# Kernel tuning notes

Hardware: AMD Instinct MI355X
Metric: run time of the kernel (lower is better)

The kernel has to match this reference:

```python
import jax, jax.numpy as jnp
import numpy as np

D_MODEL = 768
D_STATE = 16
GRID = 3
B, L = 2, 2048


def setup_inputs() -> dict:
    key = jax.random.key(0)
    ks = jax.random.split(key, 16)
    d, n, g = D_MODEL, D_STATE, GRID
    s = lambda fan: 1.0 / np.sqrt(fan)
    return {
        "x": jax.random.normal(ks[0], (B, L, d), jnp.float32),
        "priority_map": jax.random.uniform(ks[1], (B, L), jnp.float32),
        "W_in": jax.random.normal(ks[2], (d, 2 * d), jnp.float32) * s(d),
        "b_in": jnp.zeros((2 * d,), jnp.float32),
        "ln_g": jnp.ones((d,), jnp.float32),
        "ln_b": jnp.zeros((d,), jnp.float32),
        "kd_base": jax.random.normal(ks[3], (d, d), jnp.float32) * s(d),
        "kd_spline": jax.random.normal(ks[4], (d, g, d), jnp.float32) * s(d * g),
        "kb_base": jax.random.normal(ks[5], (d, n), jnp.float32) * s(d),
        "kb_spline": jax.random.normal(ks[6], (d, g, n), jnp.float32) * s(d * g),
        "kc_base": jax.random.normal(ks[7], (d, n), jnp.float32) * s(d),
        "kc_spline": jax.random.normal(ks[8], (d, g, n), jnp.float32) * s(d * g),
        "A_log": jax.random.uniform(ks[9], (d, n), jnp.float32, 1.0, 5.0),
        "D_param": jnp.ones((d,), jnp.float32),
        "W_out": jax.random.normal(ks[10], (d, d), jnp.float32) * s(d),
        "b_out": jnp.zeros((d,), jnp.float32),
    }


def _kan_dense(x, w_base, w_spline, grid):
    # FastKAN-style: SiLU base branch + Gaussian-RBF spline branch over grid_size centers.
    base = jnp.einsum("bld,do->blo", jax.nn.silu(x), w_base)
    phi = jnp.exp(-((x[..., None] - grid) ** 2))          # [B,L,D,G]
    spline = jnp.einsum("bldg,dgo->blo", phi, w_spline)
    return base + spline


def _layernorm(x, g, b, eps=1e-5):
    mu = jnp.mean(x, axis=-1, keepdims=True)
    var = jnp.mean((x - mu) ** 2, axis=-1, keepdims=True)
    return (x - mu) * jax.lax.rsqrt(var + eps) * g + b


def reference(x, priority_map, W_in, b_in, ln_g, ln_b, kd_base, kd_spline,
              kb_base, kb_spline, kc_base, kc_spline, A_log, D_param, W_out, b_out):
    grid = jnp.linspace(-1.0, 1.0, GRID).astype(x.dtype)
    xz = x @ W_in + b_in
    x_proj, z = jnp.split(xz, 2, axis=-1)                  # [B,L,D] each
    x_norm = _layernorm(x_proj, ln_g, ln_b)

    delta = jax.nn.softplus(_kan_dense(x_norm, kd_base, kd_spline, grid))  # [B,L,D]
    delta = delta * jnp.exp(-priority_map)[..., None]      # inverse priority modulation

    Bmat = _kan_dense(x_norm, kb_base, kb_spline, grid)    # [B,L,N]
    Cmat = _kan_dense(x_norm, kc_base, kc_spline, grid)    # [B,L,N]

    A_cont = -jnp.exp(A_log)                               # [D,N]
    dA = jnp.exp(jnp.einsum("bld,dn->bldn", delta, A_cont))       # [B,L,D,N]
    dBx = jnp.einsum("bld,bln->bldn", delta, Bmat) * x_proj[..., None]

    def combine(c1, c2):
        a1, b1 = c1
        a2, b2 = c2
        return a1 * a2, a2 * b1 + b2

    _, h = jax.lax.associative_scan(combine, (dA, dBx), axis=1)    # h: [B,L,D,N]

    y = jnp.einsum("bln,bldn->bld", Cmat, h) + D_param * x_proj
    y = y * jax.nn.silu(z)
    return y @ W_out + b_out
```

## Files before the change

### kernel.cpp

```cpp
#include <hip/hip_runtime.h>
#include <math.h>
#include <stdint.h>

#define D_MODEL 768
#define D_STATE 16
#define BB      2
#define LL      2048
#define MM      (BB * LL)
#define NC      64
#define CL      (LL / NC)
#define SLD     896

typedef __attribute__((ext_vector_type(8))) short short8;
typedef __attribute__((ext_vector_type(4))) float f32x4;

__device__ __forceinline__ short f2bf(float f) {
    union { float f; uint32_t u; } v; v.f = f;
    uint32_t r = v.u + 0x7fff + ((v.u >> 16) & 1);
    return (short)(r >> 16);
}
__device__ __forceinline__ float silu(float x) {
    return x / (1.0f + __expf(-x));
}

#define LDK 40

__global__ __launch_bounds__(256)
void gemm_bf16(const short* __restrict__ A,
               const short* __restrict__ Bt,
               const float* __restrict__ bias,
               const float* __restrict__ prio,
               float* __restrict__ C,
               int M, int N, int K)
{
    __shared__ short As[128 * LDK];
    __shared__ short Bs[128 * LDK];

    int tid  = threadIdx.x;
    int wid  = tid >> 6, lane = tid & 63;
    int wr   = wid >> 1, wc = wid & 1;
    int row0 = blockIdx.y * 128;
    int col0 = blockIdx.x * 128;

    f32x4 acc[4][4] = {};

    int fr = lane & 15;
    int kb = (lane >> 4) * 8;

    for (int k0 = 0; k0 < K; k0 += 32) {
        short8 av[2], bv[2];
        #pragma unroll
        for (int e = 0; e < 2; ++e) {
            int flat = tid + e * 256;
            int r  = flat >> 2;
            int cc = (flat & 3) * 8;
            av[e] = *(const short8*)(A  + (size_t)(row0 + r) * K + k0 + cc);
            bv[e] = *(const short8*)(Bt + (size_t)(col0 + r) * K + k0 + cc);
        }
        __syncthreads();
        #pragma unroll
        for (int e = 0; e < 2; ++e) {
            int flat = tid + e * 256;
            int r  = flat >> 2;
            int cc = (flat & 3) * 8;
            *(short8*)(&As[r * LDK + cc]) = av[e];
            *(short8*)(&Bs[r * LDK + cc]) = bv[e];
        }
        __syncthreads();

        short8 af[4], bf[4];
        #pragma unroll
        for (int m = 0; m < 4; ++m)
            af[m] = *(const short8*)(&As[(wr * 64 + m * 16 + fr) * LDK + kb]);
        #pragma unroll
        for (int n = 0; n < 4; ++n)
            bf[n] = *(const short8*)(&Bs[(wc * 64 + n * 16 + fr) * LDK + kb]);
        #pragma unroll
        for (int m = 0; m < 4; ++m)
            #pragma unroll
            for (int n = 0; n < 4; ++n)
                acc[m][n] = __builtin_amdgcn_mfma_f32_16x16x32_bf16(
                                af[m], bf[n], acc[m][n], 0, 0, 0);
    }

    int rq = lane >> 4;
    #pragma unroll
    for (int m = 0; m < 4; ++m) {
        #pragma unroll
        for (int n = 0; n < 4; ++n) {
            int col = col0 + wc * 64 + n * 16 + fr;
            float bvv = bias ? bias[col] : 0.0f;
            #pragma unroll
            for (int r = 0; r < 4; ++r) {
                int row = row0 + wr * 64 + m * 16 + rq * 4 + r;
                float v = acc[m][n][r] + bvv;
                if (prio && col < D_MODEL) {
                    float sp = (v > 20.0f) ? v : log1pf(__expf(v));
                    v = sp * __expf(-prio[row]);
                }
                C[(size_t)row * N + col] = v;
            }
        }
    }
}

__global__ void convert_kernel(const float* __restrict__ in, short* __restrict__ out, int n)
{
    int i = blockIdx.x * 256 + threadIdx.x;
    if (i < n) out[i] = f2bf(in[i]);
}

__global__ void wtrans_kernel(const float* __restrict__ W, short* __restrict__ Wt, int K, int N)
{
    int idx = blockIdx.x * 256 + threadIdx.x;
    if (idx >= K * N) return;
    int n = idx / K, k = idx - n * K;
    Wt[idx] = f2bf(W[(size_t)k * N + n]);
}

__global__ void repackT_kernel(const float* __restrict__ kd_b, const float* __restrict__ kd_s,
                               const float* __restrict__ kb_b, const float* __restrict__ kb_s,
                               const float* __restrict__ kc_b, const float* __restrict__ kc_s,
                               short* __restrict__ WcatT)
{
    int idx = blockIdx.x * 256 + threadIdx.x;
    if (idx >= SLD * 3072) return;
    int o = idx / 3072;
    int f = idx - o * 3072;
    float v;
    if (o >= 800) v = 0.0f;
    else if (f < D_MODEL) {
        if (o < 768)      v = kd_b[(size_t)f * 768 + o];
        else if (o < 784) v = kb_b[(size_t)f * 16 + (o - 768)];
        else              v = kc_b[(size_t)f * 16 + (o - 784)];
    } else {
        int sidx = f - D_MODEL;
        if (o < 768)      v = kd_s[(size_t)sidx * 768 + o];
        else if (o < 784) v = kb_s[(size_t)sidx * 16 + (o - 768)];
        else              v = kc_s[(size_t)sidx * 16 + (o - 784)];
    }
    WcatT[idx] = f2bf(v);
}

__global__ void ln_aug_kernel(const float* __restrict__ xz,
                              const float* __restrict__ gamma,
                              const float* __restrict__ beta,
                              short* __restrict__ Aug)
{
    int row = blockIdx.x;
    const float* xp = xz + (size_t)row * (2 * D_MODEL);
    int tid  = threadIdx.x;
    int lane = tid & 63, wave = tid >> 6;

    float v[3];
    float s = 0.f, s2 = 0.f;
    #pragma unroll
    for (int e = 0; e < 3; ++e) {
        v[e] = xp[tid + e * 256];
        s  += v[e];
        s2 += v[e] * v[e];
    }
    #pragma unroll
    for (int off = 32; off >= 1; off >>= 1) {
        s  += __shfl_xor(s,  off);
        s2 += __shfl_xor(s2, off);
    }
    __shared__ float red[2][4];
    if (lane == 0) { red[0][wave] = s; red[1][wave] = s2; }
    __syncthreads();
    s  = red[0][0] + red[0][1] + red[0][2] + red[0][3];
    s2 = red[1][0] + red[1][1] + red[1][2] + red[1][3];

    const float inv = 1.0f / (float)D_MODEL;
    float mean = s * inv;
    float var  = s2 * inv - mean * mean;
    float rstd = rsqrtf(var + 1e-5f);

    short* ar = Aug + (size_t)row * 3072;
    #pragma unroll
    for (int e = 0; e < 3; ++e) {
        int c = tid + e * 256;
        float xn = (v[e] - mean) * rstd * gamma[c] + beta[c];
        ar[c] = f2bf(silu(xn));
        #pragma unroll
        for (int g = 0; g < 3; ++g) {
            float t = xn - (float)(g - 1);
            ar[768 + 3 * c + g] = f2bf(__expf(-t * t));
        }
    }
}

__global__ __launch_bounds__(256)
void scan_phase1(const float* __restrict__ S,
                 const float* __restrict__ xz,
                 const float* __restrict__ A_log,
                 float* __restrict__ chunkA,
                 float* __restrict__ chunkH)
{
    int blk  = blockIdx.x;
    int b    = blk / (NC * 3);
    int rem  = blk % (NC * 3);
    int c    = rem / 3;
    int dblk = rem % 3;
    int d    = dblk * 256 + threadIdx.x;

    float Ac[16], h[16], P[16];
    #pragma unroll
    for (int n = 0; n < 16; ++n) {
        Ac[n] = -__expf(A_log[(size_t)d * 16 + n]);
        h[n] = 0.0f;
        P[n] = 1.0f;
    }

    int l0 = c * CL;
    for (int l = 0; l < CL; ++l) {
        int row = b * LL + l0 + l;
        const float* sr = S + (size_t)row * SLD;
        float delta = sr[d];
        float xp    = xz[(size_t)row * 1536 + d];
        float bx    = delta * xp;
        float4 B0 = *(const float4*)(sr + 768);
        float4 B1 = *(const float4*)(sr + 772);
        float4 B2 = *(const float4*)(sr + 776);
        float4 B3 = *(const float4*)(sr + 780);
        float Bv[16] = {B0.x,B0.y,B0.z,B0.w, B1.x,B1.y,B1.z,B1.w,
                        B2.x,B2.y,B2.z,B2.w, B3.x,B3.y,B3.z,B3.w};
        #pragma unroll
        for (int n = 0; n < 16; ++n) {
            float dA = __expf(delta * Ac[n]);
            h[n] = dA * h[n] + bx * Bv[n];
            P[n] *= dA;
        }
    }

    size_t base = (size_t)(b * NC + c) * (16 * 768) + d;
    #pragma unroll
    for (int n = 0; n < 16; ++n) {
        chunkA[base + n * 768] = P[n];
        chunkH[base + n * 768] = h[n];
    }
}

__global__ void scan_phase2(const float* __restrict__ chunkA,
                            const float* __restrict__ chunkH,
                            float* __restrict__ carry)
{
    int g = blockIdx.x * 256 + threadIdx.x;
    if (g >= BB * 16 * 768) return;
    int b  = g / (16 * 768);
    int nd = g % (16 * 768);

    float h0 = 0.0f;
    for (int c = 0; c < NC; ++c) {
        size_t idx = (size_t)(b * NC + c) * (16 * 768) + nd;
        float a = chunkA[idx];
        float hh = chunkH[idx];
        carry[idx] = h0;
        h0 = a * h0 + hh;
    }
}

__global__ __launch_bounds__(256)
void scan_phase3(const float* __restrict__ S,
                 const float* __restrict__ xz,
                 const float* __restrict__ A_log,
                 const float* __restrict__ Dp,
                 const float* __restrict__ carry,
                 short* __restrict__ yg)
{
    int blk  = blockIdx.x;
    int b    = blk / (NC * 3);
    int rem  = blk % (NC * 3);
    int c    = rem / 3;
    int dblk = rem % 3;
    int d    = dblk * 256 + threadIdx.x;

    float Ac[16], h[16];
    size_t base = (size_t)(b * NC + c) * (16 * 768) + d;
    #pragma unroll
    for (int n = 0; n < 16; ++n) {
        Ac[n] = -__expf(A_log[(size_t)d * 16 + n]);
        h[n]  = carry[base + n * 768];
    }
    float Dv = Dp[d];

    int l0 = c * CL;
    for (int l = 0; l < CL; ++l) {
        int row = b * LL + l0 + l;
        const float* sr = S + (size_t)row * SLD;
        float delta = sr[d];
        float xp    = xz[(size_t)row * 1536 + d];
        float bx    = delta * xp;
        float4 B0 = *(const float4*)(sr + 768);
        float4 B1 = *(const float4*)(sr + 772);
        float4 B2 = *(const float4*)(sr + 776);
        float4 B3 = *(const float4*)(sr + 780);
        float4 C0 = *(const float4*)(sr + 784);
        float4 C1 = *(const float4*)(sr + 788);
        float4 C2 = *(const float4*)(sr + 792);
        float4 C3 = *(const float4*)(sr + 796);
        float Bv[16] = {B0.x,B0.y,B0.z,B0.w, B1.x,B1.y,B1.z,B1.w,
                        B2.x,B2.y,B2.z,B2.w, B3.x,B3.y,B3.z,B3.w};
        float Cv[16] = {C0.x,C0.y,C0.z,C0.w, C1.x,C1.y,C1.z,C1.w,
                        C2.x,C2.y,C2.z,C2.w, C3.x,C3.y,C3.z,C3.w};

        float acc = Dv * xp;
        #pragma unroll
        for (int n = 0; n < 16; ++n) {
            float dA = __expf(delta * Ac[n]);
            h[n] = dA * h[n] + bx * Bv[n];
            acc += Cv[n] * h[n];
        }
        float z = xz[(size_t)row * 1536 + 768 + d];
        yg[(size_t)row * 768 + d] = f2bf(acc * silu(z));
    }
}

extern "C" void kernel_launch(void* const* d_in, const int* in_sizes, int n_in,
                              void* d_out, int out_size, void* d_ws, size_t ws_size,
                              hipStream_t stream)
{
    const float* x        = (const float*)d_in[0];
    const float* prio     = (const float*)d_in[1];
    const float* W_in     = (const float*)d_in[2];
    const float* b_in     = (const float*)d_in[3];
    const float* ln_g     = (const float*)d_in[4];
    const float* ln_b     = (const float*)d_in[5];
    const float* kd_base  = (const float*)d_in[6];
    const float* kd_spl   = (const float*)d_in[7];
    const float* kb_base  = (const float*)d_in[8];
    const float* kb_spl   = (const float*)d_in[9];
    const float* kc_base  = (const float*)d_in[10];
    const float* kc_spl   = (const float*)d_in[11];
    const float* A_log    = (const float*)d_in[12];
    const float* D_param  = (const float*)d_in[13];
    const float* W_out    = (const float*)d_in[14];
    const float* b_out    = (const float*)d_in[15];
    float* out = (float*)d_out;

    float* ws    = (float*)d_ws;
    float* xz    = ws;
    float* S     = ws + 6291456;
    float* AB    = ws + 9961472;
    short* xb    = (short*)AB;
    short* Aug   = (short*)AB;
    float* cA    = AB;
    float* cH    = AB + 1572864;
    float* cc    = AB + 3145728;
    short* yg    = (short*)(AB + 4718592);
    short* WinT  = (short*)(ws + 16252928);
    short* WcatT = (short*)(ws + 16842752);
    short* WoutT = (short*)(ws + 18219008);

    convert_kernel<<<(MM * D_MODEL + 255) / 256, 256, 0, stream>>>(x, xb, MM * D_MODEL);
    wtrans_kernel<<<(768 * 1536 + 255) / 256, 256, 0, stream>>>(W_in, WinT, 768, 1536);
    repackT_kernel<<<(SLD * 3072 + 255) / 256, 256, 0, stream>>>(
        kd_base, kd_spl, kb_base, kb_spl, kc_base, kc_spl, WcatT);
    wtrans_kernel<<<(768 * 768 + 255) / 256, 256, 0, stream>>>(W_out, WoutT, 768, 768);

    gemm_bf16<<<dim3(1536 / 128, MM / 128), 256, 0, stream>>>(
        xb, WinT, b_in, nullptr, xz, MM, 1536, 768);

    ln_aug_kernel<<<MM, 256, 0, stream>>>(xz, ln_g, ln_b, Aug);

    gemm_bf16<<<dim3(SLD / 128, MM / 128), 256, 0, stream>>>(
        Aug, WcatT, nullptr, prio, S, MM, SLD, 3072);

    scan_phase1<<<BB * NC * 3, 256, 0, stream>>>(S, xz, A_log, cA, cH);
    scan_phase2<<<(BB * 16 * 768 + 255) / 256, 256, 0, stream>>>(cA, cH, cc);
    scan_phase3<<<BB * NC * 3, 256, 0, stream>>>(S, xz, A_log, D_param, cc, yg);

    gemm_bf16<<<dim3(768 / 128, MM / 128), 256, 0, stream>>>(
        yg, WoutT, b_out, nullptr, out, MM, 768, 768);
}
```

Before: 339.9 us.

## Shrink GEMM tiles to 64x64 and load tiles directly into LDS

Rewrites the bf16 MFMA GEMM to use 64x64 output tiles per block, so each wave computes a 2x2 set of 16x16 fragments instead of 4x4. The manual register-staged copy from global to shared memory is replaced by global_load_lds builtins that write straight into LDS, removing the register round-trip. The smaller tiles launch four times as many blocks, which helps fill the GPU for these modest GEMM sizes. In exchange there is less data reuse per block, the LDS rows are unpadded (possible bank conflicts), and there is no double-buffering.

```diff
diff --git a/kernel.cpp b/kernel.cpp
--- a/kernel.cpp
+++ b/kernel.cpp
@@ -23,8 +23,6 @@
     return x / (1.0f + __expf(-x));
 }
 
-#define LDK 40
-
 __global__ __launch_bounds__(256)
 void gemm_bf16(const short* __restrict__ A,
                const short* __restrict__ Bt,
@@ -33,66 +31,57 @@
                float* __restrict__ C,
                int M, int N, int K)
 {
-    __shared__ short As[128 * LDK];
-    __shared__ short Bs[128 * LDK];
+    __shared__ short As[64 * 32];
+    __shared__ short Bs[64 * 32];
 
     int tid  = threadIdx.x;
     int wid  = tid >> 6, lane = tid & 63;
     int wr   = wid >> 1, wc = wid & 1;
-    int row0 = blockIdx.y * 128;
-    int col0 = blockIdx.x * 128;
-
-    f32x4 acc[4][4] = {};
+    int row0 = blockIdx.y * 64;
+    int col0 = blockIdx.x * 64;
+
+    int sr_ = wid * 16 + (lane >> 2);
+    int sc_ = (lane & 3) * 8;
+    const short* gA = A  + (size_t)(row0 + sr_) * K + sc_;
+    const short* gB = Bt + (size_t)(col0 + sr_) * K + sc_;
+    short* lA = As + wid * 512;
+    short* lB = Bs + wid * 512;
 
     int fr = lane & 15;
-    int kb = (lane >> 4) * 8;
+    int kg = lane >> 4;
+    f32x4 acc[2][2] = {};
 
     for (int k0 = 0; k0 < K; k0 += 32) {
-        short8 av[2], bv[2];
+        __syncthreads();
+        __builtin_amdgcn_global_load_lds(
+            (const __attribute__((address_space(1))) void*)(gA + k0),
+            (__attribute__((address_space(3))) void*)lA, 16, 0, 0);
+        __builtin_amdgcn_global_load_lds(
+            (const __attribute__((address_space(1))) void*)(gB + k0),
+            (__attribute__((address_space(3))) void*)lB, 16, 0, 0);
+        __syncthreads();
+
+        short8 af0 = *(const short8*)(&As[(wr * 32 +      fr) * 32 + kg * 8]);
+        short8 af1 = *(const short8*)(&As[(wr * 32 + 16 + fr) * 32 + kg * 8]);
+        short8 bf0 = *(const short8*)(&Bs[(wc * 32 +      fr) * 32 + kg * 8]);
+        short8 bf1 = *(const short8*)(&Bs[(wc * 32 + 16 + fr) * 32 + kg * 8]);
+
+        acc[0][0] = __builtin_amdgcn_mfma_f32_16x16x32_bf16(af0, bf0, acc[0][0], 0, 0, 0);
+        acc[0][1] = __builtin_amdgcn_mfma_f32_16x16x32_bf16(af0, bf1, acc[0][1], 0, 0, 0);
+        acc[1][0] = __builtin_amdgcn_mfma_f32_16x16x32_bf16(af1, bf0, acc[1][0], 0, 0, 0);
+        acc[1][1] = __builtin_amdgcn_mfma_f32_16x16x32_bf16(af1, bf1, acc[1][1], 0, 0, 0);
+    }
+
+    int rq = lane >> 4;
+    #pragma unroll
+    for (int m = 0; m < 2; ++m) {
         #pragma unroll
-        for (int e = 0; e < 2; ++e) {
-            int flat = tid + e * 256;
-            int r  = flat >> 2;
-            int cc = (flat & 3) * 8;
-            av[e] = *(const short8*)(A  + (size_t)(row0 + r) * K + k0 + cc);
-            bv[e] = *(const short8*)(Bt + (size_t)(col0 + r) * K + k0 + cc);
-        }
-        __syncthreads();
-        #pragma unroll
-        for (int e = 0; e < 2; ++e) {
-            int flat = tid + e * 256;
-            int r  = flat >> 2;
-            int cc = (flat & 3) * 8;
-            *(short8*)(&As[r * LDK + cc]) = av[e];
-            *(short8*)(&Bs[r * LDK + cc]) = bv[e];
-        }
-        __syncthreads();
-
-        short8 af[4], bf[4];
-        #pragma unroll
-        for (int m = 0; m < 4; ++m)
-            af[m] = *(const short8*)(&As[(wr * 64 + m * 16 + fr) * LDK + kb]);
-        #pragma unroll
-        for (int n = 0; n < 4; ++n)
-            bf[n] = *(const short8*)(&Bs[(wc * 64 + n * 16 + fr) * LDK + kb]);
-        #pragma unroll
-        for (int m = 0; m < 4; ++m)
-            #pragma unroll
-            for (int n = 0; n < 4; ++n)
-                acc[m][n] = __builtin_amdgcn_mfma_f32_16x16x32_bf16(
-                                af[m], bf[n], acc[m][n], 0, 0, 0);
-    }
-
-    int rq = lane >> 4;
-    #pragma unroll
-    for (int m = 0; m < 4; ++m) {
-        #pragma unroll
-        for (int n = 0; n < 4; ++n) {
-            int col = col0 + wc * 64 + n * 16 + fr;
+        for (int n = 0; n < 2; ++n) {
+            int col = col0 + wc * 32 + n * 16 + fr;
             float bvv = bias ? bias[col] : 0.0f;
             #pragma unroll
             for (int r = 0; r < 4; ++r) {
-                int row = row0 + wr * 64 + m * 16 + rq * 4 + r;
+                int row = row0 + wr * 32 + m * 16 + rq * 4 + r;
                 float v = acc[m][n][r] + bvv;
                 if (prio && col < D_MODEL) {
                     float sp = (v > 20.0f) ? v : log1pf(__expf(v));
@@ -358,18 +347,18 @@
         kd_base, kd_spl, kb_base, kb_spl, kc_base, kc_spl, WcatT);
     wtrans_kernel<<<(768 * 768 + 255) / 256, 256, 0, stream>>>(W_out, WoutT, 768, 768);
 
-    gemm_bf16<<<dim3(1536 / 128, MM / 128), 256, 0, stream>>>(
+    gemm_bf16<<<dim3(1536 / 64, MM / 64), 256, 0, stream>>>(
         xb, WinT, b_in, nullptr, xz, MM, 1536, 768);
 
     ln_aug_kernel<<<MM, 256, 0, stream>>>(xz, ln_g, ln_b, Aug);
 
-    gemm_bf16<<<dim3(SLD / 128, MM / 128), 256, 0, stream>>>(
+    gemm_bf16<<<dim3(SLD / 64, MM / 64), 256, 0, stream>>>(
         Aug, WcatT, nullptr, prio, S, MM, SLD, 3072);
 
     scan_phase1<<<BB * NC * 3, 256, 0, stream>>>(S, xz, A_log, cA, cH);
     scan_phase2<<<(BB * 16 * 768 + 255) / 256, 256, 0, stream>>>(cA, cH, cc);
     scan_phase3<<<BB * NC * 3, 256, 0, stream>>>(S, xz, A_log, D_param, cc, yg);
 
-    gemm_bf16<<<dim3(768 / 128, MM / 128), 256, 0, stream>>>(
+    gemm_bf16<<<dim3(768 / 64, MM / 64), 256, 0, stream>>>(
         yg, WoutT, b_out, nullptr, out, MM, 768, 768);
 }
```

Measured after the change: 306.6 us. -9.8%, faster.
